# Performance work log

Measured on AMD Instinct MI355X. Metric: run time of the kernel, lower is better.

The kernel has to match this reference:

```python
import jax, jax.numpy as jnp
import numpy as np

TAU = 1.0  # gumbel_temperature
K = 8      # number of template rows (hard-coded for SCAN)


def _forward(decodings, type_emb, w_sem, b_sem, gumbel, target_types, spans):
    B, N, M, V = decodings.shape
    # --- per-example template logits: decoder_sem[span-2][type-9](type_embedding[type]) ---
    emb = type_emb[target_types]                  # [B,H]
    w = w_sem[target_types - 9]                   # [B, K*(N+1), H]
    b = b_sem[target_types - 9]                   # [B, K*(N+1)]
    logits = (jnp.einsum('bkh,bh->bk', w, emb) + b).reshape(B, K, N + 1)
    # ragged span: only positions 0..span are valid (original views to (K, s+1))
    pos = jnp.arange(N + 1)
    valid_pos = pos[None, None, :] <= spans[:, None, None]
    logits = jnp.where(valid_pos, logits, jnp.float32(-1e30))
    logp = jax.nn.log_softmax(logits, axis=-1)
    # hard gumbel-softmax with straight-through estimator (F.gumbel_softmax hard=True)
    y_soft = jax.nn.softmax((logp + gumbel) / TAU, axis=-1)
    y_hard = jax.nn.one_hot(jnp.argmax(y_soft, -1), N + 1, dtype=y_soft.dtype)
    dt = y_hard + y_soft - jax.lax.stop_gradient(y_soft)     # [B,K,N+1]
    # special start template for target type 20: row 0 selects child 1, rest select pad (0)
    start = jax.nn.one_hot(jnp.where(jnp.arange(K) == 0, 1, 0), N + 1, dtype=dt.dtype)
    dt = jnp.where((target_types == 20)[:, None, None], start[None], dt)
    # --- apply_decoder_template ---
    pad = jnp.zeros((M, V), decodings.dtype).at[:, 0].set(1.0)  # pad vector, token 0
    choices = jnp.concatenate(
        [jnp.broadcast_to(pad[None, None], (B, 1, M, V)), decodings], axis=1)  # [B,N+1,M,V]
    out = jnp.einsum('bkn,bnmv->bkmv', dt, choices)              # [B,K,M,V]
    # per-template effective length: last position whose argmax token != 0
    out_idx = jnp.argmax(out, axis=-1)                           # [B,K,M]
    jpos = jnp.arange(M)
    lens = jnp.max(jnp.where(out_idx != 0, jpos + 1, 0), axis=-1).astype(jnp.int32)  # [B,K]
    # sequential packing of the K template outputs, clipped at M (scan over K=8)
    def step(idx, l):
        eff = jnp.minimum(l, M - idx)
        return idx + eff, (idx, eff)
    _, (offsets, effs) = jax.lax.scan(step, jnp.zeros(B, jnp.int32), lens.T)
    offsets, effs = offsets.T, effs.T                            # [B,K]
    dest = offsets[:, :, None] + jpos[None, None, :]             # [B,K,M]
    valid = jpos[None, None, :] < effs[:, :, None]
    dest = jnp.where(valid, dest, M)                             # dump invalid writes to row M
    bidx = jnp.arange(B)[:, None, None]
    vals = jnp.where(valid[..., None], out, 0.0)
    result = jnp.zeros((B, M + 1, V), decodings.dtype)
    result = result.at[bidx, dest].set(vals)
    return result[:, :M]                                         # new_d: [B,M,V]


def setup_inputs() -> dict:
    key = jax.random.key(0)
    ks = jax.random.split(key, 6)
    B, N, M, V, H, T = 256, 16, 128, 64, 128, 24
    decodings = jax.random.normal(ks[0], (B, N, M, V), jnp.float32)
    type_emb = jax.random.normal(ks[1], (T, H), jnp.float32)
    w_sem = jax.random.normal(ks[2], (T - 9, K * (N + 1), H), jnp.float32) * 0.05
    b_sem = jnp.zeros((T - 9, K * (N + 1)), jnp.float32)
    u = jax.random.uniform(ks[3], (B, K, N + 1), jnp.float32, 1e-6, 1.0 - 1e-6)
    gumbel = -jnp.log(-jnp.log(u))
    target_types = jax.random.randint(ks[4], (B,), 9, T)  # valid decoder_sem type range
    spans = jnp.full((B,), N, dtype=jnp.int32)
    return {"decodings": decodings, "type_emb": type_emb, "w_sem": w_sem,
            "b_sem": b_sem, "gumbel": gumbel, "target_types": target_types,
            "spans": spans}


def reference(decodings, type_emb, w_sem, b_sem, gumbel, target_types, spans):
    return _forward(decodings, type_emb, w_sem, b_sem, gumbel, target_types, spans)
```

## Files before the change

kernel.cpp:

```cpp
#include <hip/hip_runtime.h>

constexpr int Bn  = 256;
constexpr int Nn  = 16;
constexpr int Mn  = 128;
constexpr int Vn  = 64;
constexpr int Hn  = 128;
constexpr int Kn  = 8;
constexpr int NP1 = 17;
constexpr int KN  = Kn * NP1;

__global__ __launch_bounds__(256) void fused_template_pack(
    const float* __restrict__ dec,
    const float* __restrict__ type_emb,
    const float* __restrict__ w_sem,
    const float* __restrict__ b_sem,
    const float* __restrict__ gumbel,
    const int*   __restrict__ ttypes,
    const int*   __restrict__ spans,
    float*       __restrict__ out)
{
    const int b    = blockIdx.x;
    const int tid  = threadIdx.x;
    const int lane = tid & 63;
    const int wave = tid >> 6;

    __shared__ float s_scores[KN];
    __shared__ int   s_sel[Kn];
    __shared__ int   s_len[Kn];
    __shared__ int   s_off[Kn];
    __shared__ int   s_eff[Kn];
    __shared__ int   s_total;

    const int t    = ttypes[b];
    const int span = spans[b];

    if (t != 20) {
        if (tid < KN) {
            const int n = tid % NP1;
            float score = -1e30f;
            if (n <= span) {
                const float4* wrow = (const float4*)(w_sem + ((size_t)(t - 9) * KN + tid) * Hn);
                const float4* erow = (const float4*)(type_emb + (size_t)t * Hn);
                float acc = 0.f;
                #pragma unroll
                for (int i = 0; i < Hn / 4; ++i) {
                    float4 wv = wrow[i];
                    float4 ev = erow[i];
                    acc += wv.x * ev.x + wv.y * ev.y + wv.z * ev.z + wv.w * ev.w;
                }
                score = acc + b_sem[(t - 9) * KN + tid] + gumbel[(size_t)b * KN + tid];
            }
            s_scores[tid] = score;
        }
        __syncthreads();
        if (tid < Kn) {
            int best = 0;
            float bv = s_scores[tid * NP1];
            #pragma unroll
            for (int n = 1; n < NP1; ++n) {
                float v = s_scores[tid * NP1 + n];
                if (v > bv) { bv = v; best = n; }
            }
            s_sel[tid] = best;
        }
    } else {
        if (tid < Kn) s_sel[tid] = (tid == 0) ? 1 : 0;
    }
    __syncthreads();

    for (int k = wave; k < Kn; k += 4) {
        const int s = s_sel[k];
        int local = 0;
        if (s > 0) {
            const float* row = dec + (((size_t)b * Nn + (s - 1)) * Mn) * Vn;
            #pragma unroll
            for (int half = 0; half < 2; ++half) {
                const int m = lane + half * 64;
                const float4* p = (const float4*)(row + (size_t)m * Vn);
                float bv = -__builtin_inff();
                int bidx = 0;
                #pragma unroll
                for (int j = 0; j < Vn / 4; ++j) {
                    float4 v4 = p[j];
                    if (v4.x > bv) { bv = v4.x; bidx = 4 * j + 0; }
                    if (v4.y > bv) { bv = v4.y; bidx = 4 * j + 1; }
                    if (v4.z > bv) { bv = v4.z; bidx = 4 * j + 2; }
                    if (v4.w > bv) { bv = v4.w; bidx = 4 * j + 3; }
                }
                if (bidx != 0) local = max(local, m + 1);
            }
        }
        #pragma unroll
        for (int d = 32; d > 0; d >>= 1)
            local = max(local, __shfl_xor(local, d, 64));
        if (lane == 0) s_len[k] = local;
    }
    __syncthreads();

    if (tid == 0) {
        int idx = 0;
        #pragma unroll
        for (int k = 0; k < Kn; ++k) {
            const int eff = min(s_len[k], Mn - idx);
            s_off[k] = idx;
            s_eff[k] = eff;
            idx += eff;
        }
        s_total = idx;
    }
    __syncthreads();

    float4* outb = (float4*)(out + (size_t)b * Mn * Vn);
    for (int k = 0; k < Kn; ++k) {
        const int eff = s_eff[k];
        if (eff == 0) continue;
        const float4* src =
            (const float4*)(dec + (((size_t)b * Nn + (s_sel[k] - 1)) * Mn) * Vn);
        float4* dst = outb + (size_t)s_off[k] * (Vn / 4);
        const int cnt = eff * (Vn / 4);
        for (int i = tid; i < cnt; i += 256) dst[i] = src[i];
    }

    const int total = s_total;
    const int zcnt  = (Mn - total) * (Vn / 4);
    float4* zdst = outb + (size_t)total * (Vn / 4);
    const float4 zero = make_float4(0.f, 0.f, 0.f, 0.f);
    for (int i = tid; i < zcnt; i += 256) zdst[i] = zero;
}

extern "C" void kernel_launch(void* const* d_in, const int* in_sizes, int n_in,
                              void* d_out, int out_size, void* d_ws, size_t ws_size,
                              hipStream_t stream) {
    const float* dec      = (const float*)d_in[0];
    const float* type_emb = (const float*)d_in[1];
    const float* w_sem    = (const float*)d_in[2];
    const float* b_sem    = (const float*)d_in[3];
    const float* gumbel   = (const float*)d_in[4];
    const int*   ttypes   = (const int*)d_in[5];
    const int*   spans    = (const int*)d_in[6];
    float* out = (float*)d_out;

    fused_template_pack<<<Bn, 256, 0, stream>>>(
        dec, type_emb, w_sem, b_sem, gumbel, ttypes, spans, out);
}
```

Baseline: 191.7 us.

## Split fused kernel into per-(batch,template) select/length and pack-copy kernels

```diff
diff --git a/kernel.cpp b/kernel.cpp
--- a/kernel.cpp
+++ b/kernel.cpp
@@ -9,7 +9,7 @@
 constexpr int NP1 = 17;
 constexpr int KN  = Kn * NP1;
 
-__global__ __launch_bounds__(256) void fused_template_pack(
+__global__ __launch_bounds__(128) void select_and_len(
     const float* __restrict__ dec,
     const float* __restrict__ type_emb,
     const float* __restrict__ w_sem,
@@ -17,29 +17,31 @@
     const float* __restrict__ gumbel,
     const int*   __restrict__ ttypes,
     const int*   __restrict__ spans,
-    float*       __restrict__ out)
+    int*         __restrict__ sel_out,
+    int*         __restrict__ len_out)
 {
-    const int b    = blockIdx.x;
-    const int tid  = threadIdx.x;
+    const int bk  = blockIdx.x;
+    const int b   = bk >> 3;
+    const int k   = bk & 7;
+    const int tid = threadIdx.x;
     const int lane = tid & 63;
     const int wave = tid >> 6;
 
-    __shared__ float s_scores[KN];
-    __shared__ int   s_sel[Kn];
-    __shared__ int   s_len[Kn];
-    __shared__ int   s_off[Kn];
-    __shared__ int   s_eff[Kn];
-    __shared__ int   s_total;
+    __shared__ float s_scores[NP1];
+    __shared__ int   s_sel;
+    __shared__ int   s_wmax[2];
 
-    const int t    = ttypes[b];
-    const int span = spans[b];
+    const int t = ttypes[b];
 
-    if (t != 20) {
-        if (tid < KN) {
-            const int n = tid % NP1;
+    if (t == 20) {
+        if (tid == 0) s_sel = (k == 0) ? 1 : 0;
+    } else {
+        const int span = spans[b];
+        if (tid < NP1) {
             float score = -1e30f;
-            if (n <= span) {
-                const float4* wrow = (const float4*)(w_sem + ((size_t)(t - 9) * KN + tid) * Hn);
+            if (tid <= span) {
+                const int row = k * NP1 + tid;
+                const float4* wrow = (const float4*)(w_sem + ((size_t)(t - 9) * KN + row) * Hn);
                 const float4* erow = (const float4*)(type_emb + (size_t)t * Hn);
                 float acc = 0.f;
                 #pragma unroll
@@ -48,84 +50,84 @@
                     float4 ev = erow[i];
                     acc += wv.x * ev.x + wv.y * ev.y + wv.z * ev.z + wv.w * ev.w;
                 }
-                score = acc + b_sem[(t - 9) * KN + tid] + gumbel[(size_t)b * KN + tid];
+                score = acc + b_sem[(t - 9) * KN + row] + gumbel[(size_t)b * KN + row];
             }
             s_scores[tid] = score;
         }
         __syncthreads();
-        if (tid < Kn) {
+        if (tid == 0) {
             int best = 0;
-            float bv = s_scores[tid * NP1];
+            float bv = s_scores[0];
             #pragma unroll
             for (int n = 1; n < NP1; ++n) {
-                float v = s_scores[tid * NP1 + n];
+                float v = s_scores[n];
                 if (v > bv) { bv = v; best = n; }
             }
-            s_sel[tid] = best;
+            s_sel = best;
         }
-    } else {
-        if (tid < Kn) s_sel[tid] = (tid == 0) ? 1 : 0;
     }
     __syncthreads();
 
-    for (int k = wave; k < Kn; k += 4) {
-        const int s = s_sel[k];
-        int local = 0;
-        if (s > 0) {
-            const float* row = dec + (((size_t)b * Nn + (s - 1)) * Mn) * Vn;
-            #pragma unroll
-            for (int half = 0; half < 2; ++half) {
-                const int m = lane + half * 64;
-                const float4* p = (const float4*)(row + (size_t)m * Vn);
-                float bv = -__builtin_inff();
-                int bidx = 0;
-                #pragma unroll
-                for (int j = 0; j < Vn / 4; ++j) {
-                    float4 v4 = p[j];
-                    if (v4.x > bv) { bv = v4.x; bidx = 4 * j + 0; }
-                    if (v4.y > bv) { bv = v4.y; bidx = 4 * j + 1; }
-                    if (v4.z > bv) { bv = v4.z; bidx = 4 * j + 2; }
-                    if (v4.w > bv) { bv = v4.w; bidx = 4 * j + 3; }
-                }
-                if (bidx != 0) local = max(local, m + 1);
-            }
+    const int s = s_sel;
+    int local = 0;
+    if (s > 0) {
+        const int m = tid;
+        const float4* p = (const float4*)(dec + (((size_t)b * Nn + (s - 1)) * Mn + m) * Vn);
+        float4 v0 = p[0];
+        float mx = fmaxf(fmaxf(v0.y, v0.z), v0.w);
+        #pragma unroll
+        for (int j = 1; j < Vn / 4; ++j) {
+            float4 v = p[j];
+            mx = fmaxf(mx, fmaxf(fmaxf(v.x, v.y), fmaxf(v.z, v.w)));
         }
-        #pragma unroll
-        for (int d = 32; d > 0; d >>= 1)
-            local = max(local, __shfl_xor(local, d, 64));
-        if (lane == 0) s_len[k] = local;
+        if (mx > v0.x) local = m + 1;
     }
+    #pragma unroll
+    for (int d = 32; d > 0; d >>= 1)
+        local = max(local, __shfl_xor(local, d, 64));
+    if (lane == 0) s_wmax[wave] = local;
     __syncthreads();
+    if (tid == 0) {
+        len_out[bk] = max(s_wmax[0], s_wmax[1]);
+        sel_out[bk] = s;
+    }
+}
 
-    if (tid == 0) {
-        int idx = 0;
-        #pragma unroll
-        for (int k = 0; k < Kn; ++k) {
-            const int eff = min(s_len[k], Mn - idx);
-            s_off[k] = idx;
-            s_eff[k] = eff;
-            idx += eff;
-        }
-        s_total = idx;
+__global__ __launch_bounds__(256) void pack_copy(
+    const float* __restrict__ dec,
+    const int*   __restrict__ sel,
+    const int*   __restrict__ len,
+    float*       __restrict__ out)
+{
+    const int bk  = blockIdx.x;
+    const int b   = bk >> 3;
+    const int k   = bk & 7;
+    const int tid = threadIdx.x;
+
+    int idx = 0, myoff = 0, myeff = 0;
+    #pragma unroll
+    for (int j = 0; j < Kn; ++j) {
+        const int l = len[b * Kn + j];
+        const int e = min(l, Mn - idx);
+        if (j == k) { myoff = idx; myeff = e; }
+        idx += e;
     }
-    __syncthreads();
+    const int total = idx;
 
     float4* outb = (float4*)(out + (size_t)b * Mn * Vn);
-    for (int k = 0; k < Kn; ++k) {
-        const int eff = s_eff[k];
-        if (eff == 0) continue;
-        const float4* src =
-            (const float4*)(dec + (((size_t)b * Nn + (s_sel[k] - 1)) * Mn) * Vn);
-        float4* dst = outb + (size_t)s_off[k] * (Vn / 4);
-        const int cnt = eff * (Vn / 4);
+
+    if (myeff > 0) {
+        const int s = sel[b * Kn + k];
+        const float4* src = (const float4*)(dec + (((size_t)b * Nn + (s - 1)) * Mn) * Vn);
+        float4* dst = outb + (size_t)myoff * (Vn / 4);
+        const int cnt = myeff * (Vn / 4);
         for (int i = tid; i < cnt; i += 256) dst[i] = src[i];
     }
 
-    const int total = s_total;
-    const int zcnt  = (Mn - total) * (Vn / 4);
-    float4* zdst = outb + (size_t)total * (Vn / 4);
+    const int zcnt = (Mn - total) * (Vn / 4);
+    float4* z = outb + (size_t)total * (Vn / 4);
     const float4 zero = make_float4(0.f, 0.f, 0.f, 0.f);
-    for (int i = tid; i < zcnt; i += 256) zdst[i] = zero;
+    for (int i = tid + 256 * k; i < zcnt; i += 256 * Kn) z[i] = zero;
 }
 
 extern "C" void kernel_launch(void* const* d_in, const int* in_sizes, int n_in,
@@ -140,6 +142,10 @@
     const int*   spans    = (const int*)d_in[6];
     float* out = (float*)d_out;
 
-    fused_template_pack<<<Bn, 256, 0, stream>>>(
-        dec, type_emb, w_sem, b_sem, gumbel, ttypes, spans, out);
+    int* sel_ws = (int*)d_ws;
+    int* len_ws = sel_ws + Bn * Kn;
+
+    select_and_len<<<Bn * Kn, 128, 0, stream>>>(
+        dec, type_emb, w_sem, b_sem, gumbel, ttypes, spans, sel_ws, len_ws);
+    pack_copy<<<Bn * Kn, 256, 0, stream>>>(dec, sel_ws, len_ws, out);
 }
```

Result: slower. 206.2 us (+7.6%).

## Keep selected decoder rows in registers and copy them from registers in one pass

Applied to the files above, without the earlier changes.

```diff
diff --git a/kernel.cpp b/kernel.cpp
--- a/kernel.cpp
+++ b/kernel.cpp
@@ -9,7 +9,7 @@
 constexpr int NP1 = 17;
 constexpr int KN  = Kn * NP1;
 
-__global__ __launch_bounds__(256) void fused_template_pack(
+__global__ __launch_bounds__(1024) void fused_one_pass(
     const float* __restrict__ dec,
     const float* __restrict__ type_emb,
     const float* __restrict__ w_sem,
@@ -23,18 +23,22 @@
     const int tid  = threadIdx.x;
     const int lane = tid & 63;
     const int wave = tid >> 6;
+    const int k    = wave >> 1;
+    const int m    = ((wave & 1) << 6) | lane;
 
     __shared__ float s_scores[KN];
     __shared__ int   s_sel[Kn];
-    __shared__ int   s_len[Kn];
+    __shared__ int   s_wlen[16];
     __shared__ int   s_off[Kn];
     __shared__ int   s_eff[Kn];
     __shared__ int   s_total;
 
-    const int t    = ttypes[b];
-    const int span = spans[b];
+    const int t = ttypes[b];
 
-    if (t != 20) {
+    if (t == 20) {
+        if (tid < Kn) s_sel[tid] = (tid == 0) ? 1 : 0;
+    } else {
+        const int span = spans[b];
         if (tid < KN) {
             const int n = tid % NP1;
             float score = -1e30f;
@@ -63,69 +67,55 @@
             }
             s_sel[tid] = best;
         }
-    } else {
-        if (tid < Kn) s_sel[tid] = (tid == 0) ? 1 : 0;
     }
     __syncthreads();
 
-    for (int k = wave; k < Kn; k += 4) {
-        const int s = s_sel[k];
-        int local = 0;
-        if (s > 0) {
-            const float* row = dec + (((size_t)b * Nn + (s - 1)) * Mn) * Vn;
-            #pragma unroll
-            for (int half = 0; half < 2; ++half) {
-                const int m = lane + half * 64;
-                const float4* p = (const float4*)(row + (size_t)m * Vn);
-                float bv = -__builtin_inff();
-                int bidx = 0;
-                #pragma unroll
-                for (int j = 0; j < Vn / 4; ++j) {
-                    float4 v4 = p[j];
-                    if (v4.x > bv) { bv = v4.x; bidx = 4 * j + 0; }
-                    if (v4.y > bv) { bv = v4.y; bidx = 4 * j + 1; }
-                    if (v4.z > bv) { bv = v4.z; bidx = 4 * j + 2; }
-                    if (v4.w > bv) { bv = v4.w; bidx = 4 * j + 3; }
-                }
-                if (bidx != 0) local = max(local, m + 1);
-            }
+    const int s = s_sel[k];
+    float4 data[16];
+    int mylen = 0;
+    if (s > 0) {
+        const float4* p = (const float4*)(dec + (((size_t)b * Nn + (s - 1)) * Mn + m) * Vn);
+        #pragma unroll
+        for (int j = 0; j < Vn / 4; ++j) data[j] = p[j];
+        float mx = fmaxf(fmaxf(data[0].y, data[0].z), data[0].w);
+        #pragma unroll
+        for (int j = 1; j < Vn / 4; ++j) {
+            float4 v = data[j];
+            mx = fmaxf(mx, fmaxf(fmaxf(v.x, v.y), fmaxf(v.z, v.w)));
         }
-        #pragma unroll
-        for (int d = 32; d > 0; d >>= 1)
-            local = max(local, __shfl_xor(local, d, 64));
-        if (lane == 0) s_len[k] = local;
+        if (mx > data[0].x) mylen = m + 1;
     }
+    #pragma unroll
+    for (int d = 32; d > 0; d >>= 1)
+        mylen = max(mylen, __shfl_xor(mylen, d, 64));
+    if (lane == 0) s_wlen[wave] = mylen;
     __syncthreads();
 
     if (tid == 0) {
         int idx = 0;
         #pragma unroll
-        for (int k = 0; k < Kn; ++k) {
-            const int eff = min(s_len[k], Mn - idx);
-            s_off[k] = idx;
-            s_eff[k] = eff;
-            idx += eff;
+        for (int j = 0; j < Kn; ++j) {
+            const int l = max(s_wlen[2 * j], s_wlen[2 * j + 1]);
+            const int e = min(l, Mn - idx);
+            s_off[j] = idx;
+            s_eff[j] = e;
+            idx += e;
         }
         s_total = idx;
     }
     __syncthreads();
 
-    float4* outb = (float4*)(out + (size_t)b * Mn * Vn);
-    for (int k = 0; k < Kn; ++k) {
-        const int eff = s_eff[k];
-        if (eff == 0) continue;
-        const float4* src =
-            (const float4*)(dec + (((size_t)b * Nn + (s_sel[k] - 1)) * Mn) * Vn);
-        float4* dst = outb + (size_t)s_off[k] * (Vn / 4);
-        const int cnt = eff * (Vn / 4);
-        for (int i = tid; i < cnt; i += 256) dst[i] = src[i];
+    if (s > 0 && m < s_eff[k]) {
+        float4* dst = (float4*)(out + ((size_t)b * Mn + s_off[k] + m) * Vn);
+        #pragma unroll
+        for (int j = 0; j < Vn / 4; ++j) dst[j] = data[j];
     }
 
     const int total = s_total;
     const int zcnt  = (Mn - total) * (Vn / 4);
-    float4* zdst = outb + (size_t)total * (Vn / 4);
+    float4* z = (float4*)(out + ((size_t)b * Mn + total) * Vn);
     const float4 zero = make_float4(0.f, 0.f, 0.f, 0.f);
-    for (int i = tid; i < zcnt; i += 256) zdst[i] = zero;
+    for (int i = tid; i < zcnt; i += 1024) z[i] = zero;
 }
 
 extern "C" void kernel_launch(void* const* d_in, const int* in_sizes, int n_in,
@@ -140,6 +130,6 @@
     const int*   spans    = (const int*)d_in[6];
     float* out = (float*)d_out;
 
-    fused_template_pack<<<Bn, 256, 0, stream>>>(
+    fused_one_pass<<<Bn, 1024, 0, stream>>>(
         dec, type_emb, w_sem, b_sem, gumbel, ttypes, spans, out);
 }
```

New measurement: 192.2 us. No clear change (+0.3%).
